# Kernel tuning notes

Measured on AMD Instinct MI355X. Metric: run time of the kernel, lower is better.

The kernel has to match this reference:

```python
import jax, jax.numpy as jnp
import numpy as np
from jax import lax

NPOINT = 1024
RADIUS = 0.2
NSAMPLE = 32
BN_EPS = 1e-5


def fps(xyz, npoint):
    """Deterministic farthest point sampling (start index 0). xyz: (B,N,3) -> (B,npoint) int32."""
    B, N, _ = xyz.shape

    def step(carry, _):
        distance, farthest = carry
        centroid = jnp.take_along_axis(xyz, farthest[:, None, None], axis=1)  # (B,1,3)
        d = jnp.sum((xyz - centroid) ** 2, axis=-1)  # (B,N)
        distance = jnp.minimum(distance, d)
        nxt = jnp.argmax(distance, axis=-1).astype(jnp.int32)
        return (distance, nxt), farthest

    init = (jnp.full((B, N), jnp.inf, dtype=xyz.dtype), jnp.zeros((B,), jnp.int32))
    _, idxs = lax.scan(step, init, None, length=npoint)  # (npoint, B)
    return jnp.transpose(idxs)  # (B, npoint)


def ball_query(radius, nsample, xyz, new_xyz):
    """Deterministic ball query: first nsample in-radius indices (sorted), padded with first hit.
    xyz: (B,N,3), new_xyz: (B,S,3) -> (B,S,nsample) int32."""
    B, N, _ = xyz.shape
    # squared distances via GEMM form to avoid (B,S,N,3) intermediate
    sqr = (jnp.sum(new_xyz ** 2, -1)[:, :, None]
           + jnp.sum(xyz ** 2, -1)[:, None, :]
           - 2.0 * jnp.einsum('bsd,bnd->bsn', new_xyz, xyz))  # (B,S,N)
    idx = jnp.where(sqr <= radius ** 2, jnp.arange(N, dtype=jnp.int32), N)
    idx = jnp.sort(idx, axis=-1)[:, :, :nsample]  # (B,S,K)
    first = idx[:, :, :1]
    first = jnp.where(first == N, 0, first)  # no point in radius -> index 0
    return jnp.where(idx == N, first, idx)


def setup_inputs() -> dict:
    key = jax.random.key(0)
    ks = jax.random.split(key, 8)
    B, N, Cin = 16, 4096, 64
    xyz = jax.random.uniform(ks[0], (B, N, 3), dtype=jnp.float32)
    points = jax.random.normal(ks[1], (B, Cin, N), dtype=jnp.float32)
    chans = [Cin + 3, 64, 64, 128]
    d = {"xyz": xyz, "points": points}
    for i in range(3):
        d[f"w{i}"] = jax.random.normal(ks[2 + i], (chans[i + 1], chans[i]), dtype=jnp.float32) / np.float32(np.sqrt(chans[i]))
        d[f"g{i}"] = jnp.ones((chans[i + 1],), dtype=jnp.float32)
        d[f"b{i}"] = jnp.zeros((chans[i + 1],), dtype=jnp.float32)
    return d


def _forward(xyz, points, params):
    B, N, _ = xyz.shape
    idx = fps(xyz, NPOINT)                                     # (B,S)
    new_xyz = jnp.take_along_axis(xyz, idx[:, :, None], axis=1)  # (B,S,3)
    gidx = ball_query(RADIUS, NSAMPLE, xyz, new_xyz)             # (B,S,K)
    gather = jax.vmap(lambda p, i: p[i])
    grouped_xyz = gather(xyz, gidx) - new_xyz[:, :, None, :]     # (B,S,K,3)
    grouped_pts = gather(jnp.transpose(points, (0, 2, 1)), gidx)  # (B,S,K,C)
    feats = jnp.concatenate([grouped_xyz, grouped_pts], axis=-1)  # (B,S,K,3+C)
    for (w, g, b) in params:
        feats = jnp.einsum('oc,bskc->bsko', w, feats)
        mean = jnp.mean(feats, axis=(0, 1, 2))
        var = jnp.var(feats, axis=(0, 1, 2))
        feats = (feats - mean) * (g * lax.rsqrt(var + BN_EPS)) + b  # BatchNorm (batch stats)
        feats = jax.nn.relu(feats)
    feats = jnp.max(feats, axis=2)               # (B,S,Cout) max-pool over neighbors
    return new_xyz, jnp.transpose(feats, (0, 2, 1))  # (B,Cout,S) channel-first like torch


def reference(xyz, points, w0, g0, b0, w1, g1, b1, w2, g2, b2):
    params = [(w0, g0, b0), (w1, g1, b1), (w2, g2, b2)]
    return _forward(xyz, points, params)
```

## Files before the change

### kernel.cpp

```cpp
#include <hip/hip_runtime.h>

#define DI static __device__ __forceinline__

typedef float v2f __attribute__((ext_vector_type(2)));
typedef __attribute__((ext_vector_type(8))) short bf16x8;
typedef __attribute__((ext_vector_type(4))) float f32x4;

DI unsigned short f2bf(float f) {
  unsigned int u = __float_as_uint(f);
  u = (u + 0x7fffu + ((u >> 16) & 1u)) >> 16;
  return (unsigned short)u;
}
DI float bf2f(unsigned short h) { return __uint_as_float(((unsigned int)h) << 16); }

#define DPP_MAXU(v, ctrl)                                                      \
  {                                                                            \
    unsigned o_ = (unsigned)__builtin_amdgcn_update_dpp((int)(v), (int)(v),    \
                                                        (ctrl), 0xf, 0xf, false); \
    (v) = (o_ > (v)) ? o_ : (v);                                               \
  }
#define DPP_MINU(v, ctrl)                                                      \
  {                                                                            \
    unsigned o_ = (unsigned)__builtin_amdgcn_update_dpp((int)(v), (int)(v),    \
                                                        (ctrl), 0xf, 0xf, false); \
    (v) = (o_ < (v)) ? o_ : (v);                                               \
  }

__global__ __launch_bounds__(256) void fps_kernel(const float* __restrict__ xyz,
                                                  float* __restrict__ newxyz) {
  const int b = blockIdx.x;
  const int t = threadIdx.x;
  const int lane = t & 63, wid = t >> 6;
  const float* X = xyz + (size_t)b * 4096 * 3;
  __shared__ float XL[4096 * 3];
  __shared__ int FI[1024];
  __shared__ unsigned long long slot[2][4];
  for (int idx = t; idx < 12288; idx += 256) XL[idx] = X[idx];
  v2f px[8], py[8], pz[8], dist[8];
#pragma unroll
  for (int q = 0; q < 8; ++q) {
    int i0 = t + (q << 9);
    int i1 = i0 + 256;
    px[q] = (v2f){X[i0 * 3 + 0], X[i1 * 3 + 0]};
    py[q] = (v2f){X[i0 * 3 + 1], X[i1 * 3 + 1]};
    pz[q] = (v2f){X[i0 * 3 + 2], X[i1 * 3 + 2]};
    dist[q] = (v2f){3.402823466e38f, 3.402823466e38f};
  }
  __syncthreads();
  float cx = XL[0], cy = XL[1], cz = XL[2];
  int fi = 0;
  for (int s = 0; s < 1024; ++s) {
    if (t == 0) FI[s] = fi;
    float bv = -1.0f;
    unsigned int bi = 0;
    v2f cxv = (v2f){cx, cx}, cyv = (v2f){cy, cy}, czv = (v2f){cz, cz};
#pragma unroll
    for (int q = 0; q < 8; ++q) {
#pragma clang fp contract(off)
      v2f dx = px[q] - cxv;
      v2f dy = py[q] - cyv;
      v2f dz = pz[q] - czv;
      v2f d = (dx * dx + dy * dy) + dz * dz;
#if __has_builtin(__builtin_elementwise_min)
      v2f nd = __builtin_elementwise_min(dist[q], d);
#else
      v2f nd;
      nd.x = fminf(dist[q].x, d.x);
      nd.y = fminf(dist[q].y, d.y);
#endif
      dist[q] = nd;
      float n0 = nd.x, n1 = nd.y;
      bool c0 = (n0 > bv);
      bv = c0 ? n0 : bv;
      bi = c0 ? (unsigned)(t + (q << 9)) : bi;
      bool c1 = (n1 > bv);
      bv = c1 ? n1 : bv;
      bi = c1 ? (unsigned)(t + (q << 9) + 256) : bi;
    }
    unsigned vb = __float_as_uint(bv);
    unsigned m = vb;
    DPP_MAXU(m, 0x111);
    DPP_MAXU(m, 0x112);
    DPP_MAXU(m, 0x114);
    DPP_MAXU(m, 0x118);
    DPP_MAXU(m, 0x142);
    DPP_MAXU(m, 0x143);
    unsigned wmax = (unsigned)__builtin_amdgcn_readlane((int)m, 63);
    unsigned ik = (vb == wmax) ? bi : 0xFFFFFFFFu;
    DPP_MINU(ik, 0x111);
    DPP_MINU(ik, 0x112);
    DPP_MINU(ik, 0x114);
    DPP_MINU(ik, 0x118);
    DPP_MINU(ik, 0x142);
    DPP_MINU(ik, 0x143);
    unsigned widx = (unsigned)__builtin_amdgcn_readlane((int)ik, 63);
    const int p = s & 1;
    if (lane == 0)
      slot[p][wid] = ((unsigned long long)wmax << 32) | (unsigned long long)(~widx);
    __syncthreads();
    unsigned long long k0 = slot[p][0], k1 = slot[p][1];
    unsigned long long k2 = slot[p][2], k3 = slot[p][3];
    unsigned long long m01 = (k0 >= k1) ? k0 : k1;
    unsigned long long m23 = (k2 >= k3) ? k2 : k3;
    unsigned long long win = (m01 >= m23) ? m01 : m23;
    fi = (int)(~(unsigned int)win);
    cx = XL[fi * 3 + 0];
    cy = XL[fi * 3 + 1];
    cz = XL[fi * 3 + 2];
  }
  __syncthreads();
  float* out = newxyz + (size_t)b * 1024 * 3;
  for (int s2 = t; s2 < 1024; s2 += 256) {
    int f = FI[s2];
    out[s2 * 3 + 0] = XL[f * 3 + 0];
    out[s2 * 3 + 1] = XL[f * 3 + 1];
    out[s2 * 3 + 2] = XL[f * 3 + 2];
  }
}

__global__ __launch_bounds__(256) void p0_kernel(const float* __restrict__ points,
                                                 const float* __restrict__ w0,
                                                 float* __restrict__ P0) {
  const int b = blockIdx.x >> 6;
  const int n0 = (blockIdx.x & 63) << 6;
  const int t = threadIdx.x;
  __shared__ float W[64][64];
  for (int idx = t; idx < 4096; idx += 256) {
    int c = idx >> 6, o = idx & 63;
    W[c][o] = w0[o * 67 + 3 + c];
  }
  __syncthreads();
  const int i = t >> 4, j = t & 15;
  const float* Pb = points + (size_t)b * 64 * 4096 + n0 + 4 * i;
  float acc[4][4] = {};
  for (int c = 0; c < 64; ++c) {
    float4 xv = *(const float4*)(Pb + (size_t)c * 4096);
    float4 wv = *(const float4*)&W[c][4 * j];
    float xr[4] = {xv.x, xv.y, xv.z, xv.w};
    float wr[4] = {wv.x, wv.y, wv.z, wv.w};
#pragma unroll
    for (int rr = 0; rr < 4; ++rr)
#pragma unroll
      for (int oi = 0; oi < 4; ++oi) acc[rr][oi] = fmaf(xr[rr], wr[oi], acc[rr][oi]);
  }
#pragma unroll
  for (int rr = 0; rr < 4; ++rr) {
    float4 vv = make_float4(acc[rr][0], acc[rr][1], acc[rr][2], acc[rr][3]);
    *(float4*)(P0 + ((size_t)b * 4096 + n0 + 4 * i + rr) * 64 + 4 * j) = vv;
  }
}

__global__ __launch_bounds__(256) void ballquery_stats0_kernel(
    const float* __restrict__ xyz, const float* __restrict__ newxyz,
    const float* __restrict__ P0, const float* __restrict__ w0,
    int* __restrict__ gidx, float* __restrict__ partials0) {
  const int t = threadIdx.x;
  const int lane = t & 63, w = t >> 6;
  const int gid = blockIdx.x * 4 + w;
  const int b = gid >> 10;
  __shared__ int sel[4][32];
  __shared__ float red[4][128];
  const float* Xb = xyz + (size_t)b * 4096 * 3;
  const float cx = newxyz[(size_t)gid * 3 + 0];
  const float cy = newxyz[(size_t)gid * 3 + 1];
  const float cz = newxyz[(size_t)gid * 3 + 2];
  const float cs = __fadd_rn(__fadd_rn(__fmul_rn(cx, cx), __fmul_rn(cy, cy)), __fmul_rn(cz, cz));
  int cnt = 0, first = 0;
  bool found = false;
  for (int base = 0; base < 4096; base += 64) {
    int i = base + lane;
    float x = Xb[i * 3 + 0], y = Xb[i * 3 + 1], z = Xb[i * 3 + 2];
    float xs = __fadd_rn(__fadd_rn(__fmul_rn(x, x), __fmul_rn(y, y)), __fmul_rn(z, z));
    float dot = fmaf(cz, z, fmaf(cy, y, __fmul_rn(cx, x)));
    float sqr = __fsub_rn(__fadd_rn(cs, xs), __fmul_rn(2.0f, dot));
    bool ok = sqr <= 0.04f;
    unsigned long long mask = __ballot(ok);
    if (!found && mask != 0ull) { first = base + __builtin_ctzll(mask); found = true; }
    int pre = __popcll(mask & ((1ull << lane) - 1ull));
    int pos = cnt + pre;
    if (ok && pos < 32) sel[w][pos] = i;
    cnt += (int)__popcll(mask);
    if (cnt >= 32) break;
  }
  if (cnt < 32) {
    int pad = found ? first : 0;
    for (int p = cnt + lane; p < 32; p += 64) sel[w][p] = pad;
  }
  __syncthreads();
  if (lane < 32) gidx[(size_t)gid * 32 + lane] = sel[w][lane];
  const int c = lane;
  float wx = w0[c * 67 + 0], wy = w0[c * 67 + 1], wz = w0[c * 67 + 2];
  float ssum = 0.f, ssq = 0.f;
  const float* P0b = P0 + (size_t)b * 4096 * 64;
  for (int k = 0; k < 32; ++k) {
    int g = sel[w][k];
    float gx = Xb[g * 3 + 0] - cx, gy = Xb[g * 3 + 1] - cy, gz = Xb[g * 3 + 2] - cz;
    float a0 = fmaf(wx, gx, fmaf(wy, gy, fmaf(wz, gz, P0b[(size_t)g * 64 + c])));
    ssum += a0;
    ssq = fmaf(a0, a0, ssq);
  }
  red[w][c] = ssum;
  red[w][c + 64] = ssq;
  __syncthreads();
  if (t < 128) {
    float acc = red[0][t] + red[1][t] + red[2][t] + red[3][t];
    partials0[(size_t)t * 4096 + blockIdx.x] = acc;
  }
}

__global__ __launch_bounds__(256) void finalize_kernel(
    const float* __restrict__ partials, int C, int nblk,
    const float* __restrict__ gamma, const float* __restrict__ beta,
    float* __restrict__ scale, float* __restrict__ shift) {
  const int c = blockIdx.x, t = threadIdx.x;
  double s1 = 0.0, s2 = 0.0;
  for (int k = t; k < nblk; k += 256) {
    s1 += (double)partials[(size_t)c * nblk + k];
    s2 += (double)partials[(size_t)(C + c) * nblk + k];
  }
  __shared__ double r1[256], r2[256];
  r1[t] = s1;
  r2[t] = s2;
  __syncthreads();
  for (int off = 128; off > 0; off >>= 1) {
    if (t < off) { r1[t] += r1[t + off]; r2[t] += r2[t + off]; }
    __syncthreads();
  }
  if (t == 0) {
    const double M = 524288.0;
    double mean = r1[0] / M;
    double var = r2[0] / M - mean * mean;
    if (var < 0.0) var = 0.0;
    float sc = gamma[c] * (float)(1.0 / sqrt(var + 1e-5));
    scale[c] = sc;
    shift[c] = beta[c] - (float)mean * sc;
  }
}

__global__ __launch_bounds__(256) void p2_kernel(
    const float* __restrict__ xyz, const float* __restrict__ newxyz,
    const float* __restrict__ P0, const int* __restrict__ gidx,
    const float* __restrict__ w0, const float* __restrict__ w1,
    const float* __restrict__ sc0g, const float* __restrict__ sh0g,
    unsigned short* __restrict__ act1, float* __restrict__ partials1) {
  __shared__ unsigned short W1T[64 * 72];
  __shared__ unsigned short A[64 * 72];
  __shared__ unsigned short Cs[64 * 72];
  __shared__ float S1r[4][68], S2r[4][68];
  __shared__ float w0x[64], w0y[64], w0z[64], sc0[64], sh0[64];
  const int t = threadIdx.x;
  const int lane = t & 63, w = t >> 6;
  const int quad = lane >> 4, l15 = lane & 15;
  for (int idx = t; idx < 4096; idx += 256) {
    int o = idx >> 6, c = idx & 63;
    W1T[o * 72 + c] = f2bf(w1[o * 64 + c]);
  }
  if (t < 64) {
    w0x[t] = w0[t * 67 + 0];
    w0y[t] = w0[t * 67 + 1];
    w0z[t] = w0[t * 67 + 2];
    sc0[t] = sc0g[t];
    sh0[t] = sh0g[t];
  }
  __syncthreads();
  const int rl = t >> 2, cq = t & 3;
  float ssum[4] = {}, ssq[4] = {};
  for (int tile = 0; tile < 8; ++tile) {
    const int rowbase = (blockIdx.x * 8 + tile) << 6;
    {
      int r = rowbase + rl;
      int b = r >> 15, s = (r >> 5) & 1023;
      int g = gidx[r];
      const float* Pt = xyz + ((size_t)b * 4096 + g) * 3;
      const float* Ct = newxyz + ((size_t)b * 1024 + s) * 3;
      float dx = Pt[0] - Ct[0], dy = Pt[1] - Ct[1], dz = Pt[2] - Ct[2];
      const float4* p4 = (const float4*)(P0 + ((size_t)b * 4096 + g) * 64 + cq * 16);
      float4 a0 = p4[0], a1 = p4[1], a2 = p4[2], a3 = p4[3];
      float pv[16] = {a0.x, a0.y, a0.z, a0.w, a1.x, a1.y, a1.z, a1.w,
                      a2.x, a2.y, a2.z, a2.w, a3.x, a3.y, a3.z, a3.w};
      unsigned pk[8];
#pragma unroll
      for (int q = 0; q < 8; ++q) {
        int c0 = cq * 16 + 2 * q, c1 = c0 + 1;
        float aa = fmaf(w0x[c0], dx, fmaf(w0y[c0], dy, fmaf(w0z[c0], dz, pv[2 * q])));
        float bb = fmaf(w0x[c1], dx, fmaf(w0y[c1], dy, fmaf(w0z[c1], dz, pv[2 * q + 1])));
        float r0 = fmaxf(0.f, fmaf(aa, sc0[c0], sh0[c0]));
        float r1 = fmaxf(0.f, fmaf(bb, sc0[c1], sh0[c1]));
        pk[q] = (unsigned)f2bf(r0) | ((unsigned)f2bf(r1) << 16);
      }
      uint4* dst = (uint4*)&A[rl * 72 + cq * 16];
      dst[0] = make_uint4(pk[0], pk[1], pk[2], pk[3]);
      dst[1] = make_uint4(pk[4], pk[5], pk[6], pk[7]);
    }
    __syncthreads();
    const unsigned short* Arow = &A[(w * 16 + l15) * 72 + quad * 8];
    bf16x8 a0 = *(const bf16x8*)(Arow);
    bf16x8 a1 = *(const bf16x8*)(Arow + 32);
#pragma unroll
    for (int nt = 0; nt < 4; ++nt) {
      const unsigned short* Brow = &W1T[(nt * 16 + l15) * 72 + quad * 8];
      bf16x8 b0 = *(const bf16x8*)(Brow);
      bf16x8 b1 = *(const bf16x8*)(Brow + 32);
      f32x4 c0 = {0.f, 0.f, 0.f, 0.f};
      c0 = __builtin_amdgcn_mfma_f32_16x16x32_bf16(a0, b0, c0, 0, 0, 0);
      c0 = __builtin_amdgcn_mfma_f32_16x16x32_bf16(a1, b1, c0, 0, 0, 0);
      int o = nt * 16 + l15;
      int rloc = w * 16 + quad * 4;
#pragma unroll
      for (int reg = 0; reg < 4; ++reg) {
        float y = c0[reg];
        ssum[nt] += y;
        ssq[nt] = fmaf(y, y, ssq[nt]);
        Cs[(rloc + reg) * 72 + o] = f2bf(y);
      }
    }
    __syncthreads();
    {
      const uint4* src = (const uint4*)&Cs[rl * 72 + cq * 16];
      uint4 v0 = src[0], v1 = src[1];
      uint4* dst = (uint4*)(act1 + ((size_t)rowbase + rl) * 64 + cq * 16);
      dst[0] = v0;
      dst[1] = v1;
    }
  }
#pragma unroll
  for (int nt = 0; nt < 4; ++nt) {
    float s1 = ssum[nt];
    s1 += __shfl_xor(s1, 16, 64);
    s1 += __shfl_xor(s1, 32, 64);
    float s2 = ssq[nt];
    s2 += __shfl_xor(s2, 16, 64);
    s2 += __shfl_xor(s2, 32, 64);
    if (quad == 0) {
      S1r[w][nt * 16 + l15] = s1;
      S2r[w][nt * 16 + l15] = s2;
    }
  }
  __syncthreads();
  if (t < 64) {
    int o = t;
    float s1 = S1r[0][o] + S1r[1][o] + S1r[2][o] + S1r[3][o];
    float s2 = S2r[0][o] + S2r[1][o] + S2r[2][o] + S2r[3][o];
    partials1[(size_t)o * 1024 + blockIdx.x] = s1;
    partials1[(size_t)(64 + o) * 1024 + blockIdx.x] = s2;
  }
}

__global__ __launch_bounds__(256) void p3_kernel(
    const unsigned short* __restrict__ act1, const float* __restrict__ w2,
    const float* __restrict__ sc1g, const float* __restrict__ sh1g,
    float* __restrict__ partials2, float* __restrict__ gmx,
    float* __restrict__ gmn) {
  __shared__ unsigned short W2T[128 * 72];
  __shared__ unsigned short A[64 * 72];
  __shared__ float Mred[4][132], Nred[4][132];
  __shared__ float S1r[4][132], S2r[4][132];
  __shared__ float sc1[64], sh1[64];
  const int t = threadIdx.x;
  const int lane = t & 63, w = t >> 6;
  const int quad = lane >> 4, l15 = lane & 15;
  for (int idx = t; idx < 8192; idx += 256) {
    int o = idx >> 6, c = idx & 63;
    W2T[o * 72 + c] = f2bf(w2[o * 64 + c]);
  }
  if (t < 64) { sc1[t] = sc1g[t]; sh1[t] = sh1g[t]; }
  __syncthreads();
  const int rl = t >> 2, cq = t & 3;
  float ssum[8] = {}, ssq[8] = {};
  for (int tile = 0; tile < 8; ++tile) {
    const int rowbase = (blockIdx.x * 8 + tile) << 6;
    {
      size_t r = (size_t)rowbase + rl;
      const uint4* pr = (const uint4*)(act1 + r * 64 + cq * 16);
      uint4 aa = pr[0], bb = pr[1];
      unsigned int uu[8] = {aa.x, aa.y, aa.z, aa.w, bb.x, bb.y, bb.z, bb.w};
      unsigned int pk[8];
#pragma unroll
      for (int q = 0; q < 8; ++q) {
        int c = cq * 16 + 2 * q;
        float v0 = bf2f((unsigned short)(uu[q] & 0xffffu));
        float v1 = bf2f((unsigned short)(uu[q] >> 16));
        float r0 = fmaxf(0.f, fmaf(v0, sc1[c], sh1[c]));
        float r1 = fmaxf(0.f, fmaf(v1, sc1[c + 1], sh1[c + 1]));
        pk[q] = (unsigned)f2bf(r0) | ((unsigned)f2bf(r1) << 16);
      }
      uint4* dst = (uint4*)&A[rl * 72 + cq * 16];
      dst[0] = make_uint4(pk[0], pk[1], pk[2], pk[3]);
      dst[1] = make_uint4(pk[4], pk[5], pk[6], pk[7]);
    }
    __syncthreads();
    const unsigned short* Arow = &A[(w * 16 + l15) * 72 + quad * 8];
    bf16x8 a0 = *(const bf16x8*)(Arow);
    bf16x8 a1 = *(const bf16x8*)(Arow + 32);
    f32x4 acc[8];
#pragma unroll
    for (int nt = 0; nt < 8; ++nt) {
      const unsigned short* Brow = &W2T[(nt * 16 + l15) * 72 + quad * 8];
      bf16x8 b0 = *(const bf16x8*)(Brow);
      bf16x8 b1 = *(const bf16x8*)(Brow + 32);
      f32x4 c0 = {0.f, 0.f, 0.f, 0.f};
      c0 = __builtin_amdgcn_mfma_f32_16x16x32_bf16(a0, b0, c0, 0, 0, 0);
      c0 = __builtin_amdgcn_mfma_f32_16x16x32_bf16(a1, b1, c0, 0, 0, 0);
      acc[nt] = c0;
    }
#pragma unroll
    for (int nt = 0; nt < 8; ++nt) {
      float y0 = acc[nt][0], y1 = acc[nt][1], y2 = acc[nt][2], y3 = acc[nt][3];
      ssum[nt] += ((y0 + y1) + (y2 + y3));
      ssq[nt] = fmaf(y0, y0, ssq[nt]);
      ssq[nt] = fmaf(y1, y1, ssq[nt]);
      ssq[nt] = fmaf(y2, y2, ssq[nt]);
      ssq[nt] = fmaf(y3, y3, ssq[nt]);
      float mx = fmaxf(fmaxf(y0, y1), fmaxf(y2, y3));
      float mn = fminf(fminf(y0, y1), fminf(y2, y3));
      mx = fmaxf(mx, __shfl_xor(mx, 16, 64));
      mx = fmaxf(mx, __shfl_xor(mx, 32, 64));
      mn = fminf(mn, __shfl_xor(mn, 16, 64));
      mn = fminf(mn, __shfl_xor(mn, 32, 64));
      if (quad == 0) {
        Mred[w][nt * 16 + l15] = mx;
        Nred[w][nt * 16 + l15] = mn;
      }
    }
    __syncthreads();
    {
      int o = t & 127, g = t >> 7;
      float mx = fmaxf(Mred[2 * g][o], Mred[2 * g + 1][o]);
      float mn = fminf(Nred[2 * g][o], Nred[2 * g + 1][o]);
      int bb2 = rowbase >> 15;
      int ss2 = ((rowbase >> 5) & 1023) + g;
      size_t oidx = ((size_t)bb2 * 1024 + ss2) * 128 + o;
      gmx[oidx] = mx;
      gmn[oidx] = mn;
    }
    __syncthreads();
  }
#pragma unroll
  for (int nt = 0; nt < 8; ++nt) {
    float s1 = ssum[nt];
    s1 += __shfl_xor(s1, 16, 64);
    s1 += __shfl_xor(s1, 32, 64);
    float s2 = ssq[nt];
    s2 += __shfl_xor(s2, 16, 64);
    s2 += __shfl_xor(s2, 32, 64);
    if (quad == 0) {
      S1r[w][nt * 16 + l15] = s1;
      S2r[w][nt * 16 + l15] = s2;
    }
  }
  __syncthreads();
  if (t < 128) {
    int o = t;
    float s1 = S1r[0][o] + S1r[1][o] + S1r[2][o] + S1r[3][o];
    float s2 = S2r[0][o] + S2r[1][o] + S2r[2][o] + S2r[3][o];
    partials2[(size_t)o * 1024 + blockIdx.x] = s1;
    partials2[(size_t)(128 + o) * 1024 + blockIdx.x] = s2;
  }
}

__global__ __launch_bounds__(256) void p4f_kernel(
    const float* __restrict__ gmx, const float* __restrict__ gmn,
    const float* __restrict__ sc2g, const float* __restrict__ sh2g,
    float* __restrict__ feats) {
  __shared__ float MX[16 * 130], MN[16 * 130];
  const int t = threadIdx.x;
  const int bb = blockIdx.x >> 6;
  const int s0 = (blockIdx.x & 63) << 4;
#pragma unroll
  for (int k = 0; k < 8; ++k) {
    int idx = k * 256 + t;
    int s = idx >> 7, o = idx & 127;
    size_t g = ((size_t)bb * 1024 + s0 + s) * 128 + o;
    MX[s * 130 + o] = gmx[g];
    MN[s * 130 + o] = gmn[g];
  }
  __syncthreads();
  const int oo = t >> 1, shf = t & 1;
  const float sc = sc2g[oo], sh = sh2g[oo];
  float* dst = feats + ((size_t)bb * 128 + oo) * 1024 + s0 + shf * 8;
#pragma unroll
  for (int k = 0; k < 8; ++k) {
    int s = shf * 8 + k;
    float v = (sc >= 0.f) ? MX[s * 130 + oo] : MN[s * 130 + oo];
    dst[k] = fmaxf(0.f, fmaf(v, sc, sh));
  }
}

extern "C" void kernel_launch(void* const* d_in, const int* in_sizes, int n_in,
                              void* d_out, int out_size, void* d_ws, size_t ws_size,
                              hipStream_t stream) {
  const float* xyz = (const float*)d_in[0];
  const float* points = (const float*)d_in[1];
  const float* w0 = (const float*)d_in[2];
  const float* g0 = (const float*)d_in[3];
  const float* b0 = (const float*)d_in[4];
  const float* w1 = (const float*)d_in[5];
  const float* g1 = (const float*)d_in[6];
  const float* b1 = (const float*)d_in[7];
  const float* w2 = (const float*)d_in[8];
  const float* g2 = (const float*)d_in[9];
  const float* b2 = (const float*)d_in[10];

  float* out = (float*)d_out;
  float* newxyz = out;
  float* feats = out + 49152;

  char* ws = (char*)d_ws;
  float* P0 = (float*)ws;
  float* gmx = (float*)ws;
  float* gmn = (float*)(ws + (size_t)(8u << 20));
  int* gidx = (int*)(ws + (size_t)(16u << 20));
  unsigned short* act1 = (unsigned short*)(ws + (size_t)(18u << 20));
  float* partials0 = (float*)(ws + (size_t)(82u << 20));
  float* partials1 = (float*)(ws + (size_t)(84u << 20));
  float* partials2 = (float*)(ws + (size_t)(85u << 20));
  float* sc0 = (float*)(ws + (size_t)(86u << 20));
  float* sh0 = sc0 + 128;
  float* sc1 = sc0 + 256;
  float* sh1 = sc0 + 384;
  float* sc2 = sc0 + 512;
  float* sh2 = sc0 + 640;

  fps_kernel<<<16, 256, 0, stream>>>(xyz, newxyz);
  p0_kernel<<<1024, 256, 0, stream>>>(points, w0, P0);
  ballquery_stats0_kernel<<<4096, 256, 0, stream>>>(xyz, newxyz, P0, w0, gidx, partials0);
  finalize_kernel<<<64, 256, 0, stream>>>(partials0, 64, 4096, g0, b0, sc0, sh0);
  p2_kernel<<<1024, 256, 0, stream>>>(xyz, newxyz, P0, gidx, w0, w1, sc0, sh0, act1, partials1);
  finalize_kernel<<<64, 256, 0, stream>>>(partials1, 64, 1024, g1, b1, sc1, sh1);
  p3_kernel<<<1024, 256, 0, stream>>>(act1, w2, sc1, sh1, partials2, gmx, gmn);
  finalize_kernel<<<128, 256, 0, stream>>>(partials2, 128, 1024, g2, b2, sc2, sh2);
  p4f_kernel<<<1024, 256, 0, stream>>>(gmx, gmn, sc2, sh2, feats);
}
```

Before: 874.2 us.

## Scalarize FPS distance loop and block weight loads in p0 kernel

The FPS kernel drops its packed v2f arithmetic and uses 16 scalar registers per thread with explicit round-to-nearest ops and contiguous point ordering (t + j*256). The p0 projection kernel now preloads 16 weight rows into registers per chunk before streaming the point loads, so global loads can be issued ahead of the FMAs. The slot array gains explicit alignment. The scalar FPS path gives up packed-math throughput in exchange for a simpler dependency chain, and the register preload raises register pressure.

```diff
diff --git a/kernel.cpp b/kernel.cpp
--- a/kernel.cpp
+++ b/kernel.cpp
@@ -2,7 +2,6 @@
 
 #define DI static __device__ __forceinline__
 
-typedef float v2f __attribute__((ext_vector_type(2)));
 typedef __attribute__((ext_vector_type(8))) short bf16x8;
 typedef __attribute__((ext_vector_type(4))) float f32x4;
 
@@ -34,17 +33,16 @@
   const float* X = xyz + (size_t)b * 4096 * 3;
   __shared__ float XL[4096 * 3];
   __shared__ int FI[1024];
-  __shared__ unsigned long long slot[2][4];
+  __shared__ alignas(32) unsigned long long slot[2][4];
   for (int idx = t; idx < 12288; idx += 256) XL[idx] = X[idx];
-  v2f px[8], py[8], pz[8], dist[8];
-#pragma unroll
-  for (int q = 0; q < 8; ++q) {
-    int i0 = t + (q << 9);
-    int i1 = i0 + 256;
-    px[q] = (v2f){X[i0 * 3 + 0], X[i1 * 3 + 0]};
-    py[q] = (v2f){X[i0 * 3 + 1], X[i1 * 3 + 1]};
-    pz[q] = (v2f){X[i0 * 3 + 2], X[i1 * 3 + 2]};
-    dist[q] = (v2f){3.402823466e38f, 3.402823466e38f};
+  float px[16], py[16], pz[16], dist[16];
+#pragma unroll
+  for (int j = 0; j < 16; ++j) {
+    int i = t + (j << 8);
+    px[j] = X[i * 3 + 0];
+    py[j] = X[i * 3 + 1];
+    pz[j] = X[i * 3 + 2];
+    dist[j] = 3.402823466e38f;
   }
   __syncthreads();
   float cx = XL[0], cy = XL[1], cz = XL[2];
@@ -53,29 +51,17 @@
     if (t == 0) FI[s] = fi;
     float bv = -1.0f;
     unsigned int bi = 0;
-    v2f cxv = (v2f){cx, cx}, cyv = (v2f){cy, cy}, czv = (v2f){cz, cz};
-#pragma unroll
-    for (int q = 0; q < 8; ++q) {
-#pragma clang fp contract(off)
-      v2f dx = px[q] - cxv;
-      v2f dy = py[q] - cyv;
-      v2f dz = pz[q] - czv;
-      v2f d = (dx * dx + dy * dy) + dz * dz;
-#if __has_builtin(__builtin_elementwise_min)
-      v2f nd = __builtin_elementwise_min(dist[q], d);
-#else
-      v2f nd;
-      nd.x = fminf(dist[q].x, d.x);
-      nd.y = fminf(dist[q].y, d.y);
-#endif
-      dist[q] = nd;
-      float n0 = nd.x, n1 = nd.y;
-      bool c0 = (n0 > bv);
-      bv = c0 ? n0 : bv;
-      bi = c0 ? (unsigned)(t + (q << 9)) : bi;
-      bool c1 = (n1 > bv);
-      bv = c1 ? n1 : bv;
-      bi = c1 ? (unsigned)(t + (q << 9) + 256) : bi;
+#pragma unroll
+    for (int j = 0; j < 16; ++j) {
+      float dx = __fsub_rn(px[j], cx);
+      float dy = __fsub_rn(py[j], cy);
+      float dz = __fsub_rn(pz[j], cz);
+      float d = __fadd_rn(__fadd_rn(__fmul_rn(dx, dx), __fmul_rn(dy, dy)), __fmul_rn(dz, dz));
+      float nd = fminf(dist[j], d);
+      dist[j] = nd;
+      bool better = (nd > bv);
+      bv = better ? nd : bv;
+      bi = better ? (unsigned)(t + (j << 8)) : bi;
     }
     unsigned vb = __float_as_uint(bv);
     unsigned m = vb;
@@ -133,15 +119,23 @@
   const int i = t >> 4, j = t & 15;
   const float* Pb = points + (size_t)b * 64 * 4096 + n0 + 4 * i;
   float acc[4][4] = {};
-  for (int c = 0; c < 64; ++c) {
-    float4 xv = *(const float4*)(Pb + (size_t)c * 4096);
-    float4 wv = *(const float4*)&W[c][4 * j];
-    float xr[4] = {xv.x, xv.y, xv.z, xv.w};
-    float wr[4] = {wv.x, wv.y, wv.z, wv.w};
-#pragma unroll
-    for (int rr = 0; rr < 4; ++rr)
-#pragma unroll
-      for (int oi = 0; oi < 4; ++oi) acc[rr][oi] = fmaf(xr[rr], wr[oi], acc[rr][oi]);
+  for (int ch = 0; ch < 4; ++ch) {
+    float wr[16][4];
+#pragma unroll
+    for (int cc = 0; cc < 16; ++cc) {
+      float4 wv = *(const float4*)&W[ch * 16 + cc][4 * j];
+      wr[cc][0] = wv.x; wr[cc][1] = wv.y; wr[cc][2] = wv.z; wr[cc][3] = wv.w;
+    }
+#pragma unroll
+    for (int cc = 0; cc < 16; ++cc) {
+      int c = ch * 16 + cc;
+      float4 xv = *(const float4*)(Pb + (size_t)c * 4096);
+      float xr[4] = {xv.x, xv.y, xv.z, xv.w};
+#pragma unroll
+      for (int rr = 0; rr < 4; ++rr)
+#pragma unroll
+        for (int oi = 0; oi < 4; ++oi) acc[rr][oi] = fmaf(xr[rr], wr[cc][oi], acc[rr][oi]);
+    }
   }
 #pragma unroll
   for (int rr = 0; rr < 4; ++rr) {
```

After: 901.7 us. 1.03x slower.
